# Kernel tuning notes

Hardware: AMD Instinct MI355X
Metric: run time of the kernel (lower is better)

## Reference

```python
import jax, jax.numpy as jnp
import numpy as np
import math

D = 1024
H = 16
NEG = -10000.0


def _layernorm(x, g, b, eps=1e-6):
    mu = x.mean(-1, keepdims=True)
    var = ((x - mu) ** 2).mean(-1, keepdims=True)
    return (x - mu) / jnp.sqrt(var + eps) * g + b


def _gelu(x):
    return x * 0.5 * (1.0 + jax.lax.erf(x / math.sqrt(2.0)))


def _split_heads(x):
    N, L, _ = x.shape
    return x.reshape(N, L, H, D // H).transpose(0, 2, 1, 3)  # (N,H,L,d)


def _attention(q, k, v, mask):
    # q,k,v: (N,Lq/Lk,D); mask: (N,1,Lq,Lk) of 0/1 or None
    d = D // H
    qh, kh, vh = _split_heads(q), _split_heads(k), _split_heads(v)
    scores = jnp.einsum('bhqd,bhkd->bhqk', qh, kh) / math.sqrt(d)
    if mask is not None:
        scores = scores + (1.0 - mask) * NEG
    probs = jax.nn.softmax(scores, axis=-1)
    ctx = jnp.einsum('bhqk,bhkd->bhqd', probs, vh)
    N, _, Lq, _ = ctx.shape
    ctx = ctx.transpose(0, 2, 1, 3).reshape(N, Lq, D)
    return ctx, scores.mean(1)  # attention_vis = masked scaled scores averaged over heads


def setup_inputs() -> dict:
    key = jax.random.key(0)
    ks = jax.random.split(key, 16)
    N, Lt, Lv = 16, 512, 512
    w = lambda k: (jax.random.normal(k, (D, D), jnp.float32) * 0.02)
    inp = {
        'dec_hidden_states': jax.random.normal(ks[0], (N, Lt, D), jnp.float32),
        'dec_mask': jnp.ones((N, Lt), jnp.float32),
        'enc_outputs': jax.random.normal(ks[1], (N, Lv, D), jnp.float32),
        'sa_wq': w(ks[2]), 'sa_bq': jnp.zeros((D,), jnp.float32),
        'sa_wk': w(ks[3]), 'sa_bk': jnp.zeros((D,), jnp.float32),
        'sa_wv': w(ks[4]), 'sa_bv': jnp.zeros((D,), jnp.float32),
        'n1_g': jnp.ones((D,), jnp.float32), 'n1_b': jnp.zeros((D,), jnp.float32),
        'ca_wq': w(ks[5]), 'ca_bq': jnp.zeros((D,), jnp.float32),
        'ca_wk': w(ks[6]), 'ca_bk': jnp.zeros((D,), jnp.float32),
        'ca_wv': w(ks[7]), 'ca_bv': jnp.zeros((D,), jnp.float32),
        'n2_g': jnp.ones((D,), jnp.float32), 'n2_b': jnp.zeros((D,), jnp.float32),
        'int_w': w(ks[8]), 'int_b': jnp.zeros((D,), jnp.float32),
        'out_w': w(ks[9]), 'out_b': jnp.zeros((D,), jnp.float32),
        'out_g': jnp.ones((D,), jnp.float32), 'out_beta': jnp.zeros((D,), jnp.float32),
    }
    return inp


def reference(dec_hidden_states, dec_mask, enc_outputs,
              sa_wq, sa_bq, sa_wk, sa_bk, sa_wv, sa_bv, n1_g, n1_b,
              ca_wq, ca_bq, ca_wk, ca_bk, ca_wv, ca_bv, n2_g, n2_b,
              int_w, int_b, out_w, out_b, out_g, out_beta):
    x = dec_hidden_states
    N, Lt, _ = x.shape
    # causal + padding mask: (N,1,Lt) * tril(Lt,Lt) -> (N,Lt,Lt) -> (N,1,Lt,Lt)
    causal = jnp.tril(jnp.ones((Lt, Lt), x.dtype))
    self_mask = (dec_mask[:, None, :] * causal)[:, None, :, :]
    # self attention
    q = x @ sa_wq + sa_bq
    k = x @ sa_wk + sa_bk
    v = x @ sa_wv + sa_bv
    sa_ctx, _ = _attention(q, k, v, self_mask)
    h = _layernorm(sa_ctx + x, n1_g, n1_b)
    # cross attention (no mask)
    cq = h @ ca_wq + ca_bq
    ck = enc_outputs @ ca_wk + ca_bk
    cv = enc_outputs @ ca_wv + ca_bv
    ca_ctx, attention_vis = _attention(cq, ck, cv, None)
    h2 = _layernorm(h + ca_ctx, n2_g, n2_b)
    # intermediate (gelu FFN)
    inter = _gelu(h2 @ int_w + int_b)
    # Output: dense + residual(intermediate itself, as in original) + LayerNorm
    out = _layernorm(inter @ out_w + out_b + inter, out_g, out_beta)
    return out, attention_vis
```

## Files before the change

### kernel.cpp

```cpp
#include <hip/hip_runtime.h>
#include <hip/hip_bf16.h>
#include <math.h>

#define DDIM 1024
#define NH   16
#define LTOK 512
#define NBATCH 16

typedef unsigned short u16;
typedef unsigned short u16x8 __attribute__((ext_vector_type(8)));
typedef unsigned short u16x4 __attribute__((ext_vector_type(4)));
typedef __bf16 bf16x8 __attribute__((ext_vector_type(8)));
typedef float f32x4 __attribute__((ext_vector_type(4)));

typedef __attribute__((address_space(1))) void as1_void;
typedef __attribute__((address_space(3))) void as3_void;

__device__ __forceinline__ void llds16(const u16* g, u16* l) {
    __builtin_amdgcn_global_load_lds((as1_void*)g, (as3_void*)l, 16, 0, 0);
}

__device__ __forceinline__ float bf2f(u16 u) {
    unsigned v = ((unsigned)u) << 16;
    float f; __builtin_memcpy(&f, &v, 4); return f;
}
__device__ __forceinline__ u16 f2bf(float f) {
    unsigned u; __builtin_memcpy(&u, &f, 4);
    u += 0x7fffu + ((u >> 16) & 1u);
    return (u16)(u >> 16);
}

template<int MODE>
__global__ __launch_bounds__(256) void gemm_bt_kernel(
    const u16* __restrict__ A, int lda, long sA1, long sA2,
    const u16* __restrict__ B, int ldb, long sB1, long sB2,
    u16* __restrict__ C, float* __restrict__ Cf, int ldc, long sC1, long sC2,
    int M, int N, int K, int zdiv,
    const float* __restrict__ bias, float scale, int flags)
{
    constexpr int NB   = (MODE == 0) ? 1 : (MODE == 1 ? 2 : 3);
    constexpr int BUFE = 128 * 32;
    __shared__ __align__(16) u16 As[NB * BUFE];
    __shared__ __align__(16) u16 Bs[NB * BUFE];

    const int z  = blockIdx.y;
    const int zb = z / zdiv, zh = z - zb * zdiv;
    const u16* Ab = A + (long)zb * sA1 + (long)zh * sA2;
    const u16* Bb = B + (long)zb * sB1 + (long)zh * sB2;
    u16*   Cb  = C  ? C  + (long)zb * sC1 + (long)zh * sC2 : nullptr;
    float* Cfb = Cf ? Cf + (long)zb * sC1 + (long)zh * sC2 : nullptr;

    const int tilesN = N >> 7;
    const int tilesM = M >> 7;
    int tm, tn;
    if ((tilesM & 7) == 0) {
        const int xcd = blockIdx.x & 7, idx = blockIdx.x >> 3;
        const int mg  = tilesM >> 3;
        tm = ((idx % mg) << 3) | xcd;
        tn = idx / mg;
    } else {
        tm = blockIdx.x / tilesN;
        tn = blockIdx.x - tm * tilesN;
    }
    const int m0 = tm << 7, n0 = tn << 7;

    const int tid  = threadIdx.x;
    const int lane = tid & 63;
    const int wave = tid >> 6;
    const int wm = (wave & 1) << 6, wn = (wave >> 1) << 6;
    const int quad = lane >> 4, l16 = lane & 15;

    f32x4 acc[4][4];
#pragma unroll
    for (int i = 0; i < 4; i++)
#pragma unroll
        for (int j = 0; j < 4; j++) acc[i][j] = (f32x4){0.f, 0.f, 0.f, 0.f};

    const int lrA = (wave << 5) + (lane >> 2);
    const int lc  = (lane & 3) << 3;
    const u16* gA0 = Ab + (long)(m0 + lrA) * lda + lc;
    const u16* gA1 = Ab + (long)(m0 + lrA + 16) * lda + lc;
    const u16* gB0 = Bb + (long)(n0 + lrA) * ldb + lc;
    const u16* gB1 = Bb + (long)(n0 + lrA + 16) * ldb + lc;
    u16* lA0 = As + ((wave << 5) +  0) * 32;
    u16* lA1 = As + ((wave << 5) + 16) * 32;
    u16* lB0 = Bs + ((wave << 5) +  0) * 32;
    u16* lB1 = Bs + ((wave << 5) + 16) * 32;

    auto STAGE = [&](int bi, int k0) {
        llds16(gA0 + k0, lA0 + bi * BUFE);
        llds16(gA1 + k0, lA1 + bi * BUFE);
        llds16(gB0 + k0, lB0 + bi * BUFE);
        llds16(gB1 + k0, lB1 + bi * BUFE);
    };
    auto COMPUTE = [&](int bi) {
        const u16* Ac = As + bi * BUFE;
        const u16* Bc = Bs + bi * BUFE;
        bf16x8 af[4], bfr[4];
#pragma unroll
        for (int t = 0; t < 4; t++)
            af[t] = *(const bf16x8*)(Ac + (wm + t * 16 + l16) * 32 + quad * 8);
#pragma unroll
        for (int t = 0; t < 4; t++)
            bfr[t] = *(const bf16x8*)(Bc + (wn + t * 16 + l16) * 32 + quad * 8);
#pragma unroll
        for (int i = 0; i < 4; i++)
#pragma unroll
            for (int j = 0; j < 4; j++)
                acc[i][j] = __builtin_amdgcn_mfma_f32_16x16x32_bf16(
                    bfr[j], af[i], acc[i][j], 0, 0, 0);
    };

    if (MODE == 0) {
        for (int k0 = 0; k0 < K; k0 += 32) {
            __syncthreads();
            STAGE(0, k0);
            __syncthreads();
            COMPUTE(0);
        }
    } else if (MODE == 1) {
        STAGE(0, 0);
        __syncthreads();
        int cur = 0;
        for (int k0 = 0; k0 < K; k0 += 32) {
            const int nxt = cur ^ 1;
            if (k0 + 32 < K) STAGE(nxt, k0 + 32);
            COMPUTE(cur);
            __syncthreads();
            cur = nxt;
        }
    } else {
        STAGE(0, 0);
        STAGE(1, 32);
        int cur = 0;
        for (int k0 = 0; k0 < K; k0 += 32) {
            if (k0 + 32 < K) {
                asm volatile("s_waitcnt vmcnt(4) lgkmcnt(0)" ::: "memory");
            } else {
                asm volatile("s_waitcnt vmcnt(0) lgkmcnt(0)" ::: "memory");
            }
            __builtin_amdgcn_sched_barrier(0);
            __builtin_amdgcn_s_barrier();
            __builtin_amdgcn_sched_barrier(0);
            if (k0 + 64 < K) {
                int pre = cur + 2; if (pre >= 3) pre -= 3;
                STAGE(pre, k0 + 64);
            }
            COMPUTE(cur);
            cur = (cur == 2) ? 0 : cur + 1;
        }
    }

#pragma unroll
    for (int i = 0; i < 4; i++) {
        const long row = m0 + wm + i * 16 + l16;
#pragma unroll
        for (int j = 0; j < 4; j++) {
            const int col = n0 + wn + j * 16 + quad * 4;
            f32x4 bv = bias ? *(const f32x4*)(bias + col)
                            : (f32x4){0.f, 0.f, 0.f, 0.f};
            f32x4 v4;
#pragma unroll
            for (int r = 0; r < 4; r++) {
                float v = acc[i][j][r] * scale + bv[r];
                if (flags & 1)
                    v = 0.5f * v * (1.f + erff(v * 0.70710678118654752f));
                v4[r] = v;
            }
            if (Cfb) {
                *(f32x4*)(Cfb + row * ldc + col) = v4;
            } else {
                u16x4 ov;
#pragma unroll
                for (int r = 0; r < 4; r++) ov[r] = f2bf(v4[r]);
                *(u16x4*)(Cb + row * ldc + col) = ov;
            }
        }
    }
}

__global__ __launch_bounds__(256, 4) void flash_kernel(
    const u16* __restrict__ Q, const u16* __restrict__ K,
    const u16* __restrict__ VT, u16* __restrict__ O,
    const float* __restrict__ mask, int causal, int ldq, int ldk)
{
    __shared__ __align__(16) u16 Ks[128 * 72];
    __shared__ __align__(16) u16 Vs[64 * 136];
    const int tid  = threadIdx.x;
    const int wave = tid >> 6, lane = tid & 63;
    const int quad = lane >> 4, l16 = lane & 15;
    const int bh = blockIdx.x, qt = blockIdx.y, b = bh >> 4, h = bh & 15;
    const int qbase = qt * 64 + wave * 16;
    const int qrow  = qbase + l16;

    const u16* qp = Q + ((long)b * LTOK + qrow) * ldq + h * 64 + quad * 8;
    bf16x8 aq0 = *(const bf16x8*)(qp);
    bf16x8 aq1 = *(const bf16x8*)(qp + 32);

    f32x4 oacc[4];
#pragma unroll
    for (int jd = 0; jd < 4; jd++) oacc[jd] = (f32x4){0.f, 0.f, 0.f, 0.f};
    float m_st = -3.0e38f;
    float l_st = 0.f;

    const int krow = tid >> 3,       kcol = (tid & 7) << 3;
    const int vrow = tid >> 2,       vcol = (tid & 3) << 3;
    const u16* gK = K + ((long)b * LTOK + krow) * ldk + h * 64 + kcol;
    const u16* gV = VT + ((long)bh * 64 + vrow) * LTOK + vcol;

    const float C1    = 0.125f * 1.44269504088896340736f;
    const float NEGL2 = -10000.0f * 1.44269504088896340736f;

    const int nkt = causal ? ((qt * 64 + 63) >> 7) + 1 : (LTOK >> 7);

    u16x8 KR[4], VR[4];
#pragma unroll
    for (int i = 0; i < 4; i++) KR[i] = *(const u16x8*)(gK + (long)(i * 32) * ldk);
#pragma unroll
    for (int i = 0; i < 4; i++) VR[i] = *(const u16x8*)(gV + i * 32);
#pragma unroll
    for (int i = 0; i < 4; i++)
        *(u16x8*)(Ks + (i * 32 + krow) * 72 + kcol) = KR[i];
#pragma unroll
    for (int i = 0; i < 4; i++)
        *(u16x8*)(Vs + vrow * 136 + i * 32 + vcol) = VR[i];
    __syncthreads();

    for (int kt = 0; kt < nkt; kt++) {
        const int k0 = kt << 7;
        const bool more = (kt + 1 < nkt);

        if (more) {
            const int kn = k0 + 128;
#pragma unroll
            for (int i = 0; i < 4; i++)
                KR[i] = *(const u16x8*)(gK + (long)(kn + i * 32) * ldk);
#pragma unroll
            for (int i = 0; i < 4; i++)
                VR[i] = *(const u16x8*)(gV + kn + i * 32);
        }

        f32x4 s[8];
#pragma unroll
        for (int j = 0; j < 8; j++) {
            bf16x8 bk0 = *(const bf16x8*)(Ks + (j * 16 + l16) * 72 + quad * 8);
            bf16x8 bk1 = *(const bf16x8*)(Ks + (j * 16 + l16) * 72 + 32 + quad * 8);
            f32x4 z = (f32x4){0.f, 0.f, 0.f, 0.f};
            z = __builtin_amdgcn_mfma_f32_16x16x32_bf16(bk0, aq0, z, 0, 0, 0);
            s[j] = __builtin_amdgcn_mfma_f32_16x16x32_bf16(bk1, aq1, z, 0, 0, 0);
        }

        float tm0 = -3.0e38f, tm1 = -3.0e38f, tm2 = -3.0e38f, tm3 = -3.0e38f;
#pragma unroll
        for (int j = 0; j < 8; j++) {
            if (causal) {
                f32x4 m4 = *(const f32x4*)(mask + (long)b * LTOK + k0 + j * 16 + quad * 4);
#pragma unroll
                for (int r = 0; r < 4; r++) {
                    int key = k0 + j * 16 + quad * 4 + r;
                    float ad = (key <= qrow) ? fmaf(m4[r], -NEGL2, NEGL2) : NEGL2;
                    s[j][r] = fmaf(s[j][r], C1, ad);
                }
            } else {
#pragma unroll
                for (int r = 0; r < 4; r++) s[j][r] *= C1;
            }
            tm0 = fmaxf(tm0, s[j][0]); tm1 = fmaxf(tm1, s[j][1]);
            tm2 = fmaxf(tm2, s[j][2]); tm3 = fmaxf(tm3, s[j][3]);
        }
        float tmax = fmaxf(fmaxf(tm0, tm1), fmaxf(tm2, tm3));
        tmax = fmaxf(tmax, __shfl_xor(tmax, 16));
        tmax = fmaxf(tmax, __shfl_xor(tmax, 32));

        float mnew  = fmaxf(m_st, tmax);
        float alpha = __builtin_amdgcn_exp2f(m_st - mnew);
        m_st = mnew;

        float rs0 = 0.f, rs1 = 0.f, rs2 = 0.f, rs3 = 0.f;
        unsigned pk[8][2];
#pragma unroll
        for (int j = 0; j < 8; j++) {
            float p0 = __builtin_amdgcn_exp2f(s[j][0] - mnew);
            float p1 = __builtin_amdgcn_exp2f(s[j][1] - mnew);
            float p2 = __builtin_amdgcn_exp2f(s[j][2] - mnew);
            float p3 = __builtin_amdgcn_exp2f(s[j][3] - mnew);
            rs0 += p0; rs1 += p1; rs2 += p2; rs3 += p3;
            asm("v_cvt_pk_bf16_f32 %0, %1, %2" : "=v"(pk[j][0]) : "v"(p0), "v"(p1));
            asm("v_cvt_pk_bf16_f32 %0, %1, %2" : "=v"(pk[j][1]) : "v"(p2), "v"(p3));
        }
        float rsum = (rs0 + rs1) + (rs2 + rs3);
        rsum += __shfl_xor(rsum, 16);
        rsum += __shfl_xor(rsum, 32);
        l_st = l_st * alpha + rsum;

#pragma unroll
        for (int jd = 0; jd < 4; jd++) oacc[jd] *= alpha;

#pragma unroll
        for (int kk = 0; kk < 4; kk++) {
            unsigned wv[4] = { pk[2 * kk][0], pk[2 * kk][1],
                               pk[2 * kk + 1][0], pk[2 * kk + 1][1] };
            bf16x8 bp; __builtin_memcpy(&bp, wv, 16);
#pragma unroll
            for (int jd = 0; jd < 4; jd++) {
                const u16* vb = Vs + (jd * 16 + l16) * 136 + kk * 32 + quad * 4;
                u16 va[8];
                *(u16x4*)(va)     = *(const u16x4*)(vb);
                *(u16x4*)(va + 4) = *(const u16x4*)(vb + 16);
                bf16x8 av; __builtin_memcpy(&av, va, 16);
                oacc[jd] = __builtin_amdgcn_mfma_f32_16x16x32_bf16(av, bp, oacc[jd], 0, 0, 0);
            }
        }

        if (more) {
            __syncthreads();
#pragma unroll
            for (int i = 0; i < 4; i++)
                *(u16x8*)(Ks + (i * 32 + krow) * 72 + kcol) = KR[i];
#pragma unroll
            for (int i = 0; i < 4; i++)
                *(u16x8*)(Vs + vrow * 136 + i * 32 + vcol) = VR[i];
            __syncthreads();
        }
    }

    float linv = 1.f / l_st;
    long obase = ((long)b * LTOK + qrow) * DDIM + h * 64;
#pragma unroll
    for (int jd = 0; jd < 4; jd++) {
        u16x4 ov;
#pragma unroll
        for (int r = 0; r < 4; r++) ov[r] = f2bf(oacc[jd][r] * linv);
        *(u16x4*)(O + obase + jd * 16 + quad * 4) = ov;
    }
}

__global__ __launch_bounds__(256) void add_ln_kernel(
    const u16* __restrict__ a, const u16* __restrict__ b,
    const float* __restrict__ b32,
    const float* __restrict__ g, const float* __restrict__ bt,
    u16* __restrict__ o, float* __restrict__ of)
{
    long row = blockIdx.x;
    int tid = threadIdx.x;
    __shared__ float red[4];
    const u16* ar = a + row * DDIM;
    float xv[4]; float s = 0.f;
#pragma unroll
    for (int i = 0; i < 4; i++) {
        int c = tid + 256 * i;
        float sum = bf2f(ar[c]) + (b32 ? b32[row * DDIM + c] : bf2f(b[row * DDIM + c]));
        xv[i] = fminf(fmaxf(sum, -1.0e18f), 1.0e18f);
        s += xv[i];
    }
#pragma unroll
    for (int ofs = 32; ofs >= 1; ofs >>= 1) s += __shfl_xor(s, ofs);
    int wave = tid >> 6, lane = tid & 63;
    if (lane == 0) red[wave] = s;
    __syncthreads();
    float mu = (red[0] + red[1] + red[2] + red[3]) * (1.f / 1024.f);
    __syncthreads();
    float v = 0.f;
#pragma unroll
    for (int i = 0; i < 4; i++) { float d = xv[i] - mu; v += d * d; }
#pragma unroll
    for (int ofs = 32; ofs >= 1; ofs >>= 1) v += __shfl_xor(v, ofs);
    if (lane == 0) red[wave] = v;
    __syncthreads();
    float var = (red[0] + red[1] + red[2] + red[3]) * (1.f / 1024.f);
    float inv = rsqrtf(var + 1e-6f);
#pragma unroll
    for (int i = 0; i < 4; i++) {
        int c = tid + 256 * i;
        float r = (xv[i] - mu) * inv * g[c] + bt[c];
        if (of) of[row * DDIM + c] = r;
        else    o [row * DDIM + c] = f2bf(r);
    }
}

__global__ __launch_bounds__(256) void cvt_kernel(
    const float* __restrict__ src, u16* __restrict__ dst)
{
    long i = ((long)blockIdx.x * 256 + threadIdx.x) * 8;
    u16x8 o;
#pragma unroll
    for (int j = 0; j < 8; j++) o[j] = f2bf(src[i + j]);
    *(u16x8*)(dst + i) = o;
}

__global__ __launch_bounds__(256) void wt_kernel(
    const float* w0, const float* w1, const float* w2, const float* w3,
    const float* w4, const float* w5, const float* w6, const float* w7,
    u16* __restrict__ wt)
{
    const float* srcs[8] = {w0, w1, w2, w3, w4, w5, w6, w7};
    const float* w = srcs[blockIdx.z];
    u16* o = wt + (long)blockIdx.z * DDIM * DDIM;
    __shared__ u16 t[32][33];
    int tx = threadIdx.x & 31, ty = threadIdx.x >> 5;
    int c0 = blockIdx.x << 5, r0 = blockIdx.y << 5;
#pragma unroll
    for (int i = 0; i < 4; i++)
        t[ty + 8 * i][tx] = f2bf(w[(long)(r0 + ty + 8 * i) * DDIM + c0 + tx]);
    __syncthreads();
#pragma unroll
    for (int i = 0; i < 4; i++)
        o[(long)(c0 + ty + 8 * i) * DDIM + r0 + tx] = t[tx][ty + 8 * i];
}

__global__ __launch_bounds__(256) void biascat_kernel(
    const float* __restrict__ b0, const float* __restrict__ b1,
    const float* __restrict__ b2, float* __restrict__ dst)
{
    int i = blockIdx.x * 256 + threadIdx.x;
    const float* s = (i < 1024) ? b0 : (i < 2048) ? b1 : b2;
    dst[i] = s[i & 1023];
}

__global__ __launch_bounds__(256) void vtrans_kernel(
    const u16* __restrict__ v, u16* __restrict__ vt, int ldv)
{
    int bh = blockIdx.y; int b = bh >> 4, h = bh & 15;
    int k0 = blockIdx.x << 5;
    __shared__ __align__(16) u16 t[32 * 72];
    int kk = threadIdx.x >> 3, c = (threadIdx.x & 7) << 3;
    u16x8 val = *(const u16x8*)(v + ((long)b * LTOK + k0 + kk) * ldv + h * 64 + c);
    *(u16x8*)(t + kk * 72 + c) = val;
    __syncthreads();
    int dd = threadIdx.x >> 2, k2 = (threadIdx.x & 3) << 3;
    u16x8 o;
#pragma unroll
    for (int j = 0; j < 8; j++) o[j] = t[(k2 + j) * 72 + dd];
    *(u16x8*)(vt + ((long)bh * 64 + dd) * LTOK + k0 + k2) = o;
}

extern "C" void kernel_launch(void* const* d_in, const int* in_sizes, int n_in,
                              void* d_out, int out_size, void* d_ws, size_t ws_size,
                              hipStream_t stream)
{
    const float* x     = (const float*)d_in[0];
    const float* dmsk  = (const float*)d_in[1];
    const float* enc   = (const float*)d_in[2];
    const float* sa_wq = (const float*)d_in[3];  const float* sa_bq = (const float*)d_in[4];
    const float* sa_wk = (const float*)d_in[5];  const float* sa_bk = (const float*)d_in[6];
    const float* sa_wv = (const float*)d_in[7];  const float* sa_bv = (const float*)d_in[8];
    const float* n1_g  = (const float*)d_in[9];  const float* n1_b  = (const float*)d_in[10];
    const float* ca_wq = (const float*)d_in[11]; const float* ca_bq = (const float*)d_in[12];
    const float* ca_wk = (const float*)d_in[13]; const float* ca_bk = (const float*)d_in[14];
    const float* ca_wv = (const float*)d_in[15]; const float* ca_bv = (const float*)d_in[16];
    const float* n2_g  = (const float*)d_in[17]; const float* n2_b  = (const float*)d_in[18];
    const float* int_w = (const float*)d_in[19]; const float* int_b = (const float*)d_in[20];
    const float* out_w = (const float*)d_in[21]; const float* out_b = (const float*)d_in[22];
    const float* out_g = (const float*)d_in[23]; const float* out_bt= (const float*)d_in[24];

    float* outp = (float*)d_out;
    float* visp = outp + (long)NBATCH * LTOK * DDIM;

    const size_t WTB  = (size_t)8 * DDIM * DDIM * 2;
    const size_t BUF1 = (size_t)LTOK * DDIM * 2;
    int cb = 16;
    while (cb > 1 && WTB + (size_t)cb * 7 * BUF1 + 32768 > ws_size)
        cb >>= 1;

    char* ws = (char*)d_ws;
    size_t off = 0;
    auto alloc = [&](size_t bytes) -> u16* {
        u16* p = (u16*)(ws + off);
        off += (bytes + 255) & ~(size_t)255;
        return p;
    };
    u16* Xb  = alloc((size_t)cb * BUF1);
    u16* Eb  = alloc((size_t)cb * BUF1);
    u16* Q3  = alloc((size_t)cb * 3 * BUF1);
    u16* Vt  = alloc((size_t)cb * BUF1);
    u16* Cx  = alloc((size_t)cb * BUF1);
    u16* WT  = alloc(WTB);
    float* biasQKV = (float*)alloc(3072 * sizeof(float));
    float* biasKV  = (float*)alloc(2048 * sizeof(float));

    u16* Wsaq = WT + 0L * DDIM * DDIM;
    u16* Wcaq = WT + 3L * DDIM * DDIM;
    u16* Wcak = WT + 4L * DDIM * DDIM;
    u16* Wint = WT + 6L * DDIM * DDIM;
    u16* Wout = WT + 7L * DDIM * DDIM;

    auto gemm = [&](const u16* A, int lda, long sA1, long sA2,
                    const u16* B, int ldb, long sB1, long sB2,
                    u16* C, float* Cf, int ldc, long sC1, long sC2,
                    int M, int N, int K, int Z, int zdiv,
                    const float* bias, float scale, int flags) {
        int tM = M / 128, tN = N / 128;
        long total = (long)tM * tN * Z;
        dim3 g(tM * tN, Z), blk(256);
        if (total >= 1536)
            gemm_bt_kernel<0><<<g, blk, 0, stream>>>(
                A, lda, sA1, sA2, B, ldb, sB1, sB2, C, Cf, ldc, sC1, sC2,
                M, N, K, zdiv, bias, scale, flags);
        else if (total >= 1024)
            gemm_bt_kernel<1><<<g, blk, 0, stream>>>(
                A, lda, sA1, sA2, B, ldb, sB1, sB2, C, Cf, ldc, sC1, sC2,
                M, N, K, zdiv, bias, scale, flags);
        else
            gemm_bt_kernel<2><<<g, blk, 0, stream>>>(
                A, lda, sA1, sA2, B, ldb, sB1, sB2, C, Cf, ldc, sC1, sC2,
                M, N, K, zdiv, bias, scale, flags);
    };

    const long SLD = (long)LTOK * DDIM;
    const long SSC = (long)LTOK * LTOK;

    wt_kernel<<<dim3(32, 32, 8), dim3(256), 0, stream>>>(
        sa_wq, sa_wk, sa_wv, ca_wq, ca_wk, ca_wv, int_w, out_w, WT);
    biascat_kernel<<<dim3(12), dim3(256), 0, stream>>>(sa_bq, sa_bk, sa_bv, biasQKV);
    biascat_kernel<<<dim3(8),  dim3(256), 0, stream>>>(ca_bk, ca_bv, ca_bv, biasKV);

    for (int b0 = 0; b0 < NBATCH; b0 += cb) {
        const float* xc = x   + (long)b0 * SLD;
        const float* ec = enc + (long)b0 * SLD;
        const int M = cb * LTOK;
        const int Z = cb * NH;
        const int cvtg = (int)(((long)M * DDIM) / (256 * 8));

        u16* h   = Xb;
        u16* CQ  = Q3;
        u16* CKV = Q3 + (size_t)cb * LTOK * DDIM;
        u16* I   = Q3;
        u16* G   = Q3 + (size_t)cb * LTOK * DDIM;
        u16* h2  = Eb;

        cvt_kernel<<<dim3(cvtg), dim3(256), 0, stream>>>(xc, Xb);
        cvt_kernel<<<dim3(cvtg), dim3(256), 0, stream>>>(ec, Eb);

        gemm(Xb, DDIM, 0, 0, Wsaq, DDIM, 0, 0, Q3, nullptr, 3 * DDIM, 0, 0,
             M, 3 * DDIM, DDIM, 1, 1, biasQKV, 1.f, 0);
        vtrans_kernel<<<dim3(16, Z), dim3(256), 0, stream>>>(Q3 + 2 * DDIM, Vt, 3 * DDIM);

        flash_kernel<<<dim3(Z, 8), dim3(256), 0, stream>>>(
            Q3, Q3 + DDIM, Vt, Cx, dmsk + (long)b0 * LTOK, 1, 3 * DDIM, 3 * DDIM);

        add_ln_kernel<<<dim3(M), dim3(256), 0, stream>>>(
            Cx, nullptr, xc, n1_g, n1_b, h, nullptr);

        gemm(h, DDIM, 0, 0, Wcaq, DDIM, 0, 0, CQ, nullptr, DDIM, 0, 0,
             M, DDIM, DDIM, 1, 1, ca_bq, 1.f, 0);
        gemm(Eb, DDIM, 0, 0, Wcak, DDIM, 0, 0, CKV, nullptr, 2 * DDIM, 0, 0,
             M, 2 * DDIM, DDIM, 1, 1, biasKV, 1.f, 0);

        gemm(CQ, DDIM, SLD, 0, CKV, 2 * DDIM, (long)LTOK * 2 * DDIM, 0,
             nullptr, visp + (long)b0 * SSC, LTOK, SSC, 0,
             LTOK, LTOK, DDIM, cb, 1, nullptr, 1.f / 128.f, 0);

        vtrans_kernel<<<dim3(16, Z), dim3(256), 0, stream>>>(CKV + DDIM, Vt, 2 * DDIM);
        flash_kernel<<<dim3(Z, 8), dim3(256), 0, stream>>>(
            CQ, CKV, Vt, Cx, nullptr, 0, DDIM, 2 * DDIM);

        add_ln_kernel<<<dim3(M), dim3(256), 0, stream>>>(
            h, Cx, nullptr, n2_g, n2_b, h2, nullptr);

        gemm(h2, DDIM, 0, 0, Wint, DDIM, 0, 0, I, nullptr, DDIM, 0, 0,
             M, DDIM, DDIM, 1, 1, int_b, 1.f, 1);
        gemm(I, DDIM, 0, 0, Wout, DDIM, 0, 0, G, nullptr, DDIM, 0, 0,
             M, DDIM, DDIM, 1, 1, out_b, 1.f, 0);
        add_ln_kernel<<<dim3(M), dim3(256), 0, stream>>>(
            G, I, nullptr, out_g, out_bt, nullptr, outp + (long)b0 * SLD);
    }
}
```

Before: 586.3 us.

## Batch independent GEMMs into single grouped launches and drop triple-buffer mode

Introduces a GemmOp descriptor so one kernel launch can cover two independent GEMMs. The cross-attention Q and KV projections now run together, and the attention-vis score GEMM is co-launched with the FFN intermediate GEMM. The vis GEMM is moved after the second flash pass, and the intermediate buffers are reassigned to Vt and Cx so the co-launched work does not overwrite CQ and CKV. This cuts launch count and fills the GPU better with small grids, but removes the triple-buffered MODE 2 path, so small grids now fall back to double buffering.

```diff
diff --git a/kernel.cpp b/kernel.cpp
--- a/kernel.cpp
+++ b/kernel.cpp
@@ -30,39 +30,48 @@
     return (u16)(u >> 16);
 }
 
+struct GemmOp {
+    const u16* A; const u16* B; u16* C; float* Cf; const float* bias;
+    long sA1, sA2, sB1, sB2, sC1, sC2;
+    int lda, ldb, ldc, M, N, K, zdiv, flags, nblk;
+    float scale;
+};
+
 template<int MODE>
-__global__ __launch_bounds__(256) void gemm_bt_kernel(
-    const u16* __restrict__ A, int lda, long sA1, long sA2,
-    const u16* __restrict__ B, int ldb, long sB1, long sB2,
-    u16* __restrict__ C, float* __restrict__ Cf, int ldc, long sC1, long sC2,
-    int M, int N, int K, int zdiv,
-    const float* __restrict__ bias, float scale, int flags)
-{
-    constexpr int NB   = (MODE == 0) ? 1 : (MODE == 1 ? 2 : 3);
+__global__ __launch_bounds__(256) void gemm_bt_kernel(GemmOp o1, GemmOp o2)
+{
+    constexpr int NB   = (MODE == 0) ? 1 : 2;
     constexpr int BUFE = 128 * 32;
     __shared__ __align__(16) u16 As[NB * BUFE];
     __shared__ __align__(16) u16 Bs[NB * BUFE];
 
-    const int z  = blockIdx.y;
-    const int zb = z / zdiv, zh = z - zb * zdiv;
-    const u16* Ab = A + (long)zb * sA1 + (long)zh * sA2;
-    const u16* Bb = B + (long)zb * sB1 + (long)zh * sB2;
-    u16*   Cb  = C  ? C  + (long)zb * sC1 + (long)zh * sC2 : nullptr;
-    float* Cfb = Cf ? Cf + (long)zb * sC1 + (long)zh * sC2 : nullptr;
-
-    const int tilesN = N >> 7;
-    const int tilesM = M >> 7;
+    const bool second = (int)blockIdx.x >= o1.nblk;
+    const GemmOp& o = second ? o2 : o1;
+    int bidx = blockIdx.x - (second ? o1.nblk : 0);
+
+    const int tilesN = o.N >> 7;
+    const int tilesM = o.M >> 7;
+    const int tiles  = tilesM * tilesN;
+    const int z = bidx / tiles;
+    const int t = bidx - z * tiles;
+    const int zb = z / o.zdiv, zh = z - zb * o.zdiv;
+
     int tm, tn;
     if ((tilesM & 7) == 0) {
-        const int xcd = blockIdx.x & 7, idx = blockIdx.x >> 3;
+        const int xcd = t & 7, idx = t >> 3;
         const int mg  = tilesM >> 3;
         tm = ((idx % mg) << 3) | xcd;
         tn = idx / mg;
     } else {
-        tm = blockIdx.x / tilesN;
-        tn = blockIdx.x - tm * tilesN;
+        tm = t / tilesN;
+        tn = t - tm * tilesN;
     }
     const int m0 = tm << 7, n0 = tn << 7;
+
+    const u16* Ab = o.A + (long)zb * o.sA1 + (long)zh * o.sA2;
+    const u16* Bb = o.B + (long)zb * o.sB1 + (long)zh * o.sB2;
+    u16*   Cb  = o.C  ? o.C  + (long)zb * o.sC1 + (long)zh * o.sC2 : nullptr;
+    float* Cfb = o.Cf ? o.Cf + (long)zb * o.sC1 + (long)zh * o.sC2 : nullptr;
 
     const int tid  = threadIdx.x;
     const int lane = tid & 63;
@@ -78,10 +87,10 @@
 
     const int lrA = (wave << 5) + (lane >> 2);
     const int lc  = (lane & 3) << 3;
-    const u16* gA0 = Ab + (long)(m0 + lrA) * lda + lc;
-    const u16* gA1 = Ab + (long)(m0 + lrA + 16) * lda + lc;
-    const u16* gB0 = Bb + (long)(n0 + lrA) * ldb + lc;
-    const u16* gB1 = Bb + (long)(n0 + lrA + 16) * ldb + lc;
+    const u16* gA0 = Ab + (long)(m0 + lrA) * o.lda + lc;
+    const u16* gA1 = Ab + (long)(m0 + lrA + 16) * o.lda + lc;
+    const u16* gB0 = Bb + (long)(n0 + lrA) * o.ldb + lc;
+    const u16* gB1 = Bb + (long)(n0 + lrA + 16) * o.ldb + lc;
     u16* lA0 = As + ((wave << 5) +  0) * 32;
     u16* lA1 = As + ((wave << 5) + 16) * 32;
     u16* lB0 = Bs + ((wave << 5) +  0) * 32;
@@ -98,11 +107,11 @@
         const u16* Bc = Bs + bi * BUFE;
         bf16x8 af[4], bfr[4];
 #pragma unroll
-        for (int t = 0; t < 4; t++)
-            af[t] = *(const bf16x8*)(Ac + (wm + t * 16 + l16) * 32 + quad * 8);
-#pragma unroll
-        for (int t = 0; t < 4; t++)
-            bfr[t] = *(const bf16x8*)(Bc + (wn + t * 16 + l16) * 32 + quad * 8);
+        for (int t2 = 0; t2 < 4; t2++)
+            af[t2] = *(const bf16x8*)(Ac + (wm + t2 * 16 + l16) * 32 + quad * 8);
+#pragma unroll
+        for (int t2 = 0; t2 < 4; t2++)
+            bfr[t2] = *(const bf16x8*)(Bc + (wn + t2 * 16 + l16) * 32 + quad * 8);
 #pragma unroll
         for (int i = 0; i < 4; i++)
 #pragma unroll
@@ -111,6 +120,7 @@
                     bfr[j], af[i], acc[i][j], 0, 0, 0);
     };
 
+    const int K = o.K;
     if (MODE == 0) {
         for (int k0 = 0; k0 < K; k0 += 32) {
             __syncthreads();
@@ -118,7 +128,7 @@
             __syncthreads();
             COMPUTE(0);
         }
-    } else if (MODE == 1) {
+    } else {
         STAGE(0, 0);
         __syncthreads();
         int cur = 0;
@@ -129,26 +139,6 @@
             __syncthreads();
             cur = nxt;
         }
-    } else {
-        STAGE(0, 0);
-        STAGE(1, 32);
-        int cur = 0;
-        for (int k0 = 0; k0 < K; k0 += 32) {
-            if (k0 + 32 < K) {
-                asm volatile("s_waitcnt vmcnt(4) lgkmcnt(0)" ::: "memory");
-            } else {
-                asm volatile("s_waitcnt vmcnt(0) lgkmcnt(0)" ::: "memory");
-            }
-            __builtin_amdgcn_sched_barrier(0);
-            __builtin_amdgcn_s_barrier();
-            __builtin_amdgcn_sched_barrier(0);
-            if (k0 + 64 < K) {
-                int pre = cur + 2; if (pre >= 3) pre -= 3;
-                STAGE(pre, k0 + 64);
-            }
-            COMPUTE(cur);
-            cur = (cur == 2) ? 0 : cur + 1;
-        }
     }
 
 #pragma unroll
@@ -157,23 +147,23 @@
 #pragma unroll
         for (int j = 0; j < 4; j++) {
             const int col = n0 + wn + j * 16 + quad * 4;
-            f32x4 bv = bias ? *(const f32x4*)(bias + col)
-                            : (f32x4){0.f, 0.f, 0.f, 0.f};
+            f32x4 bv = o.bias ? *(const f32x4*)(o.bias + col)
+                              : (f32x4){0.f, 0.f, 0.f, 0.f};
             f32x4 v4;
 #pragma unroll
             for (int r = 0; r < 4; r++) {
-                float v = acc[i][j][r] * scale + bv[r];
-                if (flags & 1)
+                float v = acc[i][j][r] * o.scale + bv[r];
+                if (o.flags & 1)
                     v = 0.5f * v * (1.f + erff(v * 0.70710678118654752f));
                 v4[r] = v;
             }
             if (Cfb) {
-                *(f32x4*)(Cfb + row * ldc + col) = v4;
+                *(f32x4*)(Cfb + row * o.ldc + col) = v4;
             } else {
                 u16x4 ov;
 #pragma unroll
                 for (int r = 0; r < 4; r++) ov[r] = f2bf(v4[r]);
-                *(u16x4*)(Cb + row * ldc + col) = ov;
+                *(u16x4*)(Cb + row * o.ldc + col) = ov;
             }
         }
     }
@@ -484,27 +474,26 @@
     u16* Wint = WT + 6L * DDIM * DDIM;
     u16* Wout = WT + 7L * DDIM * DDIM;
 
-    auto gemm = [&](const u16* A, int lda, long sA1, long sA2,
-                    const u16* B, int ldb, long sB1, long sB2,
-                    u16* C, float* Cf, int ldc, long sC1, long sC2,
-                    int M, int N, int K, int Z, int zdiv,
-                    const float* bias, float scale, int flags) {
-        int tM = M / 128, tN = N / 128;
-        long total = (long)tM * tN * Z;
-        dim3 g(tM * tN, Z), blk(256);
-        if (total >= 1536)
-            gemm_bt_kernel<0><<<g, blk, 0, stream>>>(
-                A, lda, sA1, sA2, B, ldb, sB1, sB2, C, Cf, ldc, sC1, sC2,
-                M, N, K, zdiv, bias, scale, flags);
-        else if (total >= 1024)
-            gemm_bt_kernel<1><<<g, blk, 0, stream>>>(
-                A, lda, sA1, sA2, B, ldb, sB1, sB2, C, Cf, ldc, sC1, sC2,
-                M, N, K, zdiv, bias, scale, flags);
+    auto mkop = [](const u16* A, int lda, const u16* B, int ldb,
+                   u16* C, float* Cf, int ldc, int M, int N, int K,
+                   const float* bias, float scale, int flags) -> GemmOp {
+        GemmOp o{};
+        o.A = A; o.B = B; o.C = C; o.Cf = Cf; o.bias = bias;
+        o.sA1 = 0; o.sA2 = 0; o.sB1 = 0; o.sB2 = 0; o.sC1 = 0; o.sC2 = 0;
+        o.lda = lda; o.ldb = ldb; o.ldc = ldc; o.M = M; o.N = N; o.K = K;
+        o.zdiv = 1; o.flags = flags; o.nblk = (M / 128) * (N / 128);
+        o.scale = scale;
+        return o;
+    };
+
+    auto launch = [&](GemmOp o1, GemmOp o2) {
+        int nb = o1.nblk + o2.nblk;
+        if (nb >= 1536)
+            gemm_bt_kernel<0><<<dim3(nb), dim3(256), 0, stream>>>(o1, o2);
         else
-            gemm_bt_kernel<2><<<g, blk, 0, stream>>>(
-                A, lda, sA1, sA2, B, ldb, sB1, sB2, C, Cf, ldc, sC1, sC2,
-                M, N, K, zdiv, bias, scale, flags);
+            gemm_bt_kernel<1><<<dim3(nb), dim3(256), 0, stream>>>(o1, o2);
     };
+    GemmOp nil{};
 
     const long SLD = (long)LTOK * DDIM;
     const long SSC = (long)LTOK * LTOK;
@@ -524,15 +513,15 @@
         u16* h   = Xb;
         u16* CQ  = Q3;
         u16* CKV = Q3 + (size_t)cb * LTOK * DDIM;
-        u16* I   = Q3;
-        u16* G   = Q3 + (size_t)cb * LTOK * DDIM;
+        u16* I   = Vt;
+        u16* G   = Cx;
         u16* h2  = Eb;
 
         cvt_kernel<<<dim3(cvtg), dim3(256), 0, stream>>>(xc, Xb);
         cvt_kernel<<<dim3(cvtg), dim3(256), 0, stream>>>(ec, Eb);
 
-        gemm(Xb, DDIM, 0, 0, Wsaq, DDIM, 0, 0, Q3, nullptr, 3 * DDIM, 0, 0,
-             M, 3 * DDIM, DDIM, 1, 1, biasQKV, 1.f, 0);
+        launch(mkop(Xb, DDIM, Wsaq, DDIM, Q3, nullptr, 3 * DDIM,
+                    M, 3 * DDIM, DDIM, biasQKV, 1.f, 0), nil);
         vtrans_kernel<<<dim3(16, Z), dim3(256), 0, stream>>>(Q3 + 2 * DDIM, Vt, 3 * DDIM);
 
         flash_kernel<<<dim3(Z, 8), dim3(256), 0, stream>>>(
@@ -541,14 +530,10 @@
         add_ln_kernel<<<dim3(M), dim3(256), 0, stream>>>(
             Cx, nullptr, xc, n1_g, n1_b, h, nullptr);
 
-        gemm(h, DDIM, 0, 0, Wcaq, DDIM, 0, 0, CQ, nullptr, DDIM, 0, 0,
-             M, DDIM, DDIM, 1, 1, ca_bq, 1.f, 0);
-        gemm(Eb, DDIM, 0, 0, Wcak, DDIM, 0, 0, CKV, nullptr, 2 * DDIM, 0, 0,
-             M, 2 * DDIM, DDIM, 1, 1, biasKV, 1.f, 0);
-
-        gemm(CQ, DDIM, SLD, 0, CKV, 2 * DDIM, (long)LTOK * 2 * DDIM, 0,
-             nullptr, visp + (long)b0 * SSC, LTOK, SSC, 0,
-             LTOK, LTOK, DDIM, cb, 1, nullptr, 1.f / 128.f, 0);
+        launch(mkop(h,  DDIM, Wcaq, DDIM, CQ,  nullptr, DDIM,
+                    M, DDIM, DDIM, ca_bq, 1.f, 0),
+               mkop(Eb, DDIM, Wcak, DDIM, CKV, nullptr, 2 * DDIM,
+                    M, 2 * DDIM, DDIM, biasKV, 1.f, 0));
 
         vtrans_kernel<<<dim3(16, Z), dim3(256), 0, stream>>>(CKV + DDIM, Vt, 2 * DDIM);
         flash_kernel<<<dim3(Z, 8), dim3(256), 0, stream>>>(
@@ -557,10 +542,21 @@
         add_ln_kernel<<<dim3(M), dim3(256), 0, stream>>>(
             h, Cx, nullptr, n2_g, n2_b, h2, nullptr);
 
-        gemm(h2, DDIM, 0, 0, Wint, DDIM, 0, 0, I, nullptr, DDIM, 0, 0,
-             M, DDIM, DDIM, 1, 1, int_b, 1.f, 1);
-        gemm(I, DDIM, 0, 0, Wout, DDIM, 0, 0, G, nullptr, DDIM, 0, 0,
-             M, DDIM, DDIM, 1, 1, out_b, 1.f, 0);
+        GemmOp ovis{};
+        ovis.A = CQ;  ovis.lda = DDIM;     ovis.sA1 = SLD;               ovis.sA2 = 0;
+        ovis.B = CKV; ovis.ldb = 2 * DDIM; ovis.sB1 = (long)LTOK * 2 * DDIM; ovis.sB2 = 0;
+        ovis.C = nullptr; ovis.Cf = visp + (long)b0 * SSC;
+        ovis.ldc = LTOK; ovis.sC1 = SSC; ovis.sC2 = 0;
+        ovis.M = LTOK; ovis.N = LTOK; ovis.K = DDIM; ovis.zdiv = 1;
+        ovis.bias = nullptr; ovis.scale = 1.f / 128.f; ovis.flags = 0;
+        ovis.nblk = (LTOK / 128) * (LTOK / 128) * cb;
+        launch(ovis,
+               mkop(h2, DDIM, Wint, DDIM, I, nullptr, DDIM,
+                    M, DDIM, DDIM, int_b, 1.f, 1));
+
+        launch(mkop(I, DDIM, Wout, DDIM, G, nullptr, DDIM,
+                    M, DDIM, DDIM, out_b, 1.f, 0), nil);
+
         add_ln_kernel<<<dim3(M), dim3(256), 0, stream>>>(
             G, I, nullptr, out_g, out_bt, nullptr, outp + (long)b0 * SLD);
     }
```

New measurement: 564.0 us. -3.8%, faster.
